# Kernel tuning notes

Hardware: AMD Instinct MI355X
Metric: run time of the kernel (lower is better)

Reference implementation:

```python
import jax, jax.numpy as jnp
import numpy as np

K = 20          # neighbors per point
BN_EPS = 1e-5


def setup_inputs() -> dict:
    key = jax.random.key(0)
    k0, k1, k2 = jax.random.split(key, 3)
    B, N, C_OUT, EDGE_DIM = 8, 4096, 64, 4  # edge feat = [diff(3), ||diff||(1)]
    x = jax.random.normal(k0, (B, N, 3), dtype=jnp.float32)
    pos = jax.random.uniform(k1, (B, N, 3), dtype=jnp.float32)
    # shared 1x1-conv MLP params (Conv1d k=1 == per-edge linear) + BatchNorm affine
    W = jax.random.normal(k2, (C_OUT, EDGE_DIM), dtype=jnp.float32) * 0.1
    b = jnp.zeros((C_OUT,), jnp.float32)
    gamma = jnp.ones((C_OUT,), jnp.float32)
    beta = jnp.zeros((C_OUT,), jnp.float32)
    return {"x": x, "pos": pos, "W": W, "b": b, "gamma": gamma, "beta": beta}


def _knn_idx(pos, k):
    # pos: [B, N, 3] -> idx of k nearest neighbors per point, self excluded. [B, N, k]
    B, N, _ = pos.shape
    sq = jnp.sum(pos * pos, axis=-1)                                   # [B, N]
    d2 = sq[:, :, None] + sq[:, None, :] - 2.0 * jnp.einsum('bnd,bmd->bnm', pos, pos)
    d2 = d2 + jnp.eye(N, dtype=pos.dtype) * 1e10                       # exclude self-loop
    _, idx = jax.lax.top_k(-d2, k)                                     # [B, N, k]
    return idx


def _forward(pos, W, b, gamma, beta, k=K):
    idx = _knn_idx(pos, k)                                             # [B, N, k] (int, non-diff)
    nbr = jax.vmap(lambda p, i: p[i])(pos, idx)                        # gather: [B, N, k, 3]
    diff = nbr - pos[:, :, None, :]                                    # neighbor - center
    dist = jnp.sqrt(jnp.sum(diff * diff, axis=-1, keepdims=True))      # [B, N, k, 1]
    feat = jnp.concatenate([diff, dist], axis=-1)                      # [B, N, k, 4]
    # shared MLP (1x1 conv): per-edge linear
    y = jnp.einsum('bnkc,oc->bnko', feat, W) + b                       # [B, N, k, 64]
    # BatchNorm1d over all edges (training-mode batch stats), per channel
    mu = jnp.mean(y, axis=(0, 1, 2))
    var = jnp.var(y, axis=(0, 1, 2))
    y = (y - mu) * jax.lax.rsqrt(var + BN_EPS) * gamma + beta
    y = jax.nn.relu(y)
    y = jnp.where(y >= 0, y, 0.1 * y)   # leaky_relu(0.1) from source (no-op after relu, kept for fidelity)
    return jnp.mean(y, axis=2)          # mean pool over each node's k edges -> [B, N, 64]


def reference(x, pos, W, b, gamma, beta):
    # x only provides (batch_size, num_points) in the source; math uses pos.
    return _forward(pos, W, b, gamma, beta)
```

## Files before the change

kernel.cpp:

```cpp
#include <hip/hip_runtime.h>

#define NB    8
#define NP    4096
#define KNN   20
#define COUT  64
#define S     4
#define BLK   256
#define QPB   (BLK / S)
#define BPB   (NP / QPB)
#define NBLK1 (NB * BPB)
#define NBLK2 ((NB * NP * 4) / BLK)
#define NMOM  14
#define MSTR  16
#define LCAP  32
#define FBIG  3.402823466e38f

typedef unsigned long long u64;
typedef unsigned int u32;

__device__ __forceinline__ void ins20(float d, u32 mi,
                                      float* __restrict__ bd,
                                      u32* __restrict__ bi) {
#pragma unroll
    for (int j = KNN - 1; j >= 1; --j) {
        const bool sh  = d < bd[j - 1];
        const bool in_ = !sh && (d < bd[j]);
        bi[j] = sh ? bi[j - 1] : (in_ ? mi : bi[j]);
        bd[j] = fminf(fmaxf(bd[j - 1], d), bd[j]);
    }
    if (d < bd[0]) { bi[0] = mi; bd[0] = d; }
}

__device__ __forceinline__ float d2_of(const float4 c, const float4 q) {
    const float base = __fadd_rn(q.w, c.w);
    const float dot  = fmaf(q.z, c.z, fmaf(q.y, c.y, __fmul_rn(q.x, c.x)));
    return fmaf(-2.0f, dot, base);
}

__global__ __launch_bounds__(BLK, 2)
void knn_kernel(const float* __restrict__ pos,
                unsigned short* __restrict__ idx_out,
                float* __restrict__ mom) {
    __shared__ float4 sp[NP];

    const int b = blockIdx.x / BPB;
    const int t = threadIdx.x;
    const int s = t & (S - 1);
    const int n = (blockIdx.x % BPB) * QPB + (t >> 2);
    const float* pb = pos + (size_t)b * NP * 3;

    for (int i = t; i < NP; i += BLK) {
        const float x = pb[3 * i], y = pb[3 * i + 1], z = pb[3 * i + 2];
        const float csq = __fadd_rn(
            __fadd_rn(__fmul_rn(x, x), __fmul_rn(y, y)), __fmul_rn(z, z));
        sp[i] = make_float4(x, y, z, csq);
    }
    __syncthreads();

    const float4 q = sp[n];

    float sd0 = FBIG, sd1 = FBIG, sd2 = FBIG, sd3 = FBIG, sd4 = FBIG;
#pragma unroll 4
    for (int i = 0; i < NP / S; i += 4) {
        const int m = (i << 2) | s;
        const float d2 = d2_of(sp[m], q);
        if (m != n && d2 < sd4) {
            sd4 = fminf(fmaxf(sd3, d2), sd4);
            sd3 = fminf(fmaxf(sd2, d2), sd3);
            sd2 = fminf(fmaxf(sd1, d2), sd2);
            sd1 = fminf(fmaxf(sd0, d2), sd1);
            sd0 = fminf(sd0, d2);
        }
    }
    float gb = sd4;
    gb = fmaxf(gb, __shfl_xor(gb, 1));
    gb = fmaxf(gb, __shfl_xor(gb, 2));

    float bd[KNN];
    u32   bi[KNN];
#pragma unroll
    for (int j = 0; j < KNN; ++j) { bd[j] = FBIG; bi[j] = 0xFFFu; }
    u64 pidx = 0;
    int cnt = 0;

#pragma unroll 4
    for (int i = 0; i < NP / S; ++i) {
        const int m = (i << 2) | s;
        const float d2 = d2_of(sp[m], q);
        const bool acc = (d2 <= gb);
        pidx = acc ? ((pidx << 12) | (u64)(u32)m) : pidx;
        cnt += (int)acc;
        if (__ballot(cnt == 4)) {
            const u32 m3 = (u32)(pidx >> 36) & 0xFFFu;
            const u32 m2 = (u32)(pidx >> 24) & 0xFFFu;
            const u32 m1 = (u32)(pidx >> 12) & 0xFFFu;
            const u32 m0 = (u32)pidx & 0xFFFu;
            const float d3r = d2_of(sp[m3], q);
            const float d2r = d2_of(sp[m2], q);
            const float d1r = d2_of(sp[m1], q);
            const float d0r = d2_of(sp[m0], q);
            ins20((cnt >= 4 && m3 != (u32)n) ? d3r : FBIG, m3, bd, bi);
            ins20((cnt >= 3 && m2 != (u32)n) ? d2r : FBIG, m2, bd, bi);
            ins20((cnt >= 2 && m1 != (u32)n) ? d1r : FBIG, m1, bd, bi);
            ins20((cnt >= 1 && m0 != (u32)n) ? d0r : FBIG, m0, bd, bi);
            cnt = 0; pidx = 0;
            float g = bd[KNN - 1];
            g = fminf(g, __shfl_xor(g, 1));
            g = fminf(g, __shfl_xor(g, 2));
            float g4 = bd[4];
            g4 = fmaxf(g4, __shfl_xor(g4, 1));
            g4 = fmaxf(g4, __shfl_xor(g4, 2));
            gb = fminf(gb, fminf(g, g4));
        }
    }
    {
        const u32 m3 = (u32)(pidx >> 36) & 0xFFFu;
        const u32 m2 = (u32)(pidx >> 24) & 0xFFFu;
        const u32 m1 = (u32)(pidx >> 12) & 0xFFFu;
        const u32 m0 = (u32)pidx & 0xFFFu;
        const float d3r = d2_of(sp[m3], q);
        const float d2r = d2_of(sp[m2], q);
        const float d1r = d2_of(sp[m1], q);
        const float d0r = d2_of(sp[m0], q);
        ins20((cnt >= 4 && m3 != (u32)n) ? d3r : FBIG, m3, bd, bi);
        ins20((cnt >= 3 && m2 != (u32)n) ? d2r : FBIG, m2, bd, bi);
        ins20((cnt >= 2 && m1 != (u32)n) ? d1r : FBIG, m1, bd, bi);
        ins20((cnt >= 1 && m0 != (u32)n) ? d0r : FBIG, m0, bd, bi);
    }

    u64 key[LCAP];
#pragma unroll
    for (int j = 0; j < KNN; ++j) {
        u32 fb = __float_as_uint(bd[j]);
        fb ^= (u32)((int)fb >> 31) | 0x80000000u;
        key[j] = ((u64)fb << 12) | bi[j];
    }
#pragma unroll
    for (int j = KNN; j < LCAP; ++j) key[j] = ~0ull;

#pragma unroll
    for (int r = 1; r <= 2; r <<= 1) {
#pragma unroll
        for (int j = 0; j < LCAP / 2; ++j) {
            const int k2 = LCAP - 1 - j;
            const u64 pa = (u64)__shfl_xor((long long)key[k2], r);
            const u64 pc = (u64)__shfl_xor((long long)key[j],  r);
            key[j]  = key[j]  < pa ? key[j]  : pa;
            key[k2] = key[k2] < pc ? key[k2] : pc;
        }
#pragma unroll
        for (int d = 16; d >= 1; d >>= 1) {
#pragma unroll
            for (int j = 0; j < LCAP; ++j) {
                if ((j & d) == 0) {
                    const u64 x = key[j], y = key[j + d];
                    key[j]     = x < y ? x : y;
                    key[j + d] = x < y ? y : x;
                }
            }
        }
    }

    unsigned short* ip = idx_out + ((size_t)b * NP + n) * KNN;
    float s1x = 0, s1y = 0, s1z = 0, s1d = 0;
    float mxx = 0, mxy = 0, mxz = 0, mxd = 0;
    float myy = 0, myz = 0, myd = 0;
    float mzz = 0, mzd = 0, mdd = 0;
#pragma unroll
    for (int j = 0; j < KNN; ++j) {
        const int m = (int)(key[j] & 0xFFFull);
        if ((j & 3) == s) ip[j] = (unsigned short)m;
        const float4 c = sp[m];
        const float dx = __fsub_rn(c.x, q.x);
        const float dy = __fsub_rn(c.y, q.y);
        const float dz = __fsub_rn(c.z, q.z);
        const float dd = sqrtf(__fadd_rn(
            __fadd_rn(__fmul_rn(dx, dx), __fmul_rn(dy, dy)), __fmul_rn(dz, dz)));
        s1x += dx; s1y += dy; s1z += dz; s1d += dd;
        mxx += dx * dx; mxy += dx * dy; mxz += dx * dz; mxd += dx * dd;
        myy += dy * dy; myz += dy * dz; myd += dy * dd;
        mzz += dz * dz; mzd += dz * dd; mdd += dd * dd;
    }
    {
        float vals[NMOM] = {s1x, s1y, s1z, s1d,
                            mxx, mxy, mxz, mxd, myy, myz, myd, mzz, mzd, mdd};
#pragma unroll
        for (int tt = 0; tt < NMOM; ++tt) {
            float v = vals[tt];
#pragma unroll
            for (int off = 32; off > 0; off >>= 1) v += __shfl_down(v, off);
            if ((t & 63) == 0) atomicAdd(&mom[tt * MSTR], v * 0.25f);
        }
    }
}

__global__ __launch_bounds__(BLK)
void out_kernel(const float* __restrict__ pos,
                const float* __restrict__ W,
                const float* __restrict__ bias,
                const float* __restrict__ gamma,
                const float* __restrict__ beta,
                const unsigned short* __restrict__ idx_in,
                const float* __restrict__ mom,
                float* __restrict__ out) {
    __shared__ float sWp[COUT][4];
    __shared__ float sbp[COUT];

    if (threadIdx.x < COUT) {
        const int o = threadIdx.x;
        double S1[4], s2v[10];
#pragma unroll
        for (int tt = 0; tt < 4; ++tt)  S1[tt]  = (double)mom[tt * MSTR];
#pragma unroll
        for (int tt = 0; tt < 10; ++tt) s2v[tt] = (double)mom[(4 + tt) * MSTR];
        const double M = (double)NB * NP * KNN;
        double mean[4];
#pragma unroll
        for (int c = 0; c < 4; ++c) mean[c] = S1[c] / M;
        double E2[4][4];
        E2[0][0] = s2v[0]; E2[0][1] = E2[1][0] = s2v[1];
        E2[0][2] = E2[2][0] = s2v[2]; E2[0][3] = E2[3][0] = s2v[3];
        E2[1][1] = s2v[4]; E2[1][2] = E2[2][1] = s2v[5];
        E2[1][3] = E2[3][1] = s2v[6];
        E2[2][2] = s2v[7]; E2[2][3] = E2[3][2] = s2v[8];
        E2[3][3] = s2v[9];
        double w[4];
#pragma unroll
        for (int c = 0; c < 4; ++c) w[c] = (double)W[o * 4 + c];
        const double bo = (double)bias[o];
        double mu = bo;
#pragma unroll
        for (int c = 0; c < 4; ++c) mu += w[c] * mean[c];
        double var = 0.0;
#pragma unroll
        for (int c = 0; c < 4; ++c)
#pragma unroll
            for (int c2 = 0; c2 < 4; ++c2)
                var += w[c] * w[c2] * (E2[c][c2] / M - mean[c] * mean[c2]);
        const double scale = (double)gamma[o] / sqrt(var + 1e-5);
#pragma unroll
        for (int c = 0; c < 4; ++c) sWp[o][c] = (float)(w[c] * scale);
        sbp[o] = (float)((bo - mu) * scale + (double)beta[o]);
    }
    __syncthreads();

    const int t  = threadIdx.x;
    const int gq = blockIdx.x * (BLK / 4) + (t >> 2);
    const int b  = gq / NP, n = gq % NP;
    const int c0 = (t & 3) * 16;
    const float* pb = pos + (size_t)b * NP * 3;
    const float qx = pb[3 * n], qy = pb[3 * n + 1], qz = pb[3 * n + 2];

    float fx[KNN], fy[KNN], fz[KNN], fd[KNN];
    const unsigned short* ip = idx_in + (size_t)gq * KNN;
#pragma unroll
    for (int j = 0; j < KNN; ++j) {
        const int m = ip[j];
        const float dx = __fsub_rn(pb[3 * m], qx);
        const float dy = __fsub_rn(pb[3 * m + 1], qy);
        const float dz = __fsub_rn(pb[3 * m + 2], qz);
        fx[j] = dx; fy[j] = dy; fz[j] = dz;
        fd[j] = sqrtf(__fadd_rn(
            __fadd_rn(__fmul_rn(dx, dx), __fmul_rn(dy, dy)), __fmul_rn(dz, dz)));
    }

    float* ob = out + (size_t)gq * COUT + c0;
    const float inv = 1.0f / (float)KNN;
#pragma unroll
    for (int o = 0; o < 16; o += 4) {
        float acc[4];
#pragma unroll
        for (int qq = 0; qq < 4; ++qq) {
            const float w0 = sWp[c0 + o + qq][0], w1 = sWp[c0 + o + qq][1];
            const float w2 = sWp[c0 + o + qq][2], w3 = sWp[c0 + o + qq][3];
            const float bb = sbp[c0 + o + qq];
            float a = 0.f;
#pragma unroll
            for (int j = 0; j < KNN; ++j) {
                float y = fmaf(fx[j], w0,
                          fmaf(fy[j], w1, fmaf(fz[j], w2, fmaf(fd[j], w3, bb))));
                a += fmaxf(y, 0.f);
            }
            acc[qq] = a * inv;
        }
        float4 p = {acc[0], acc[1], acc[2], acc[3]};
        *reinterpret_cast<float4*>(ob + o) = p;
    }
}

extern "C" void kernel_launch(void* const* d_in, const int* in_sizes, int n_in,
                              void* d_out, int out_size, void* d_ws, size_t ws_size,
                              hipStream_t stream) {
    (void)in_sizes; (void)n_in; (void)out_size; (void)ws_size;
    const float* pos   = (const float*)d_in[1];
    const float* W     = (const float*)d_in[2];
    const float* bias  = (const float*)d_in[3];
    const float* gamma = (const float*)d_in[4];
    const float* beta  = (const float*)d_in[5];
    float* out = (float*)d_out;

    float* mom = (float*)d_ws;
    unsigned short* idxws = (unsigned short*)((char*)d_ws + 1024);

    hipMemsetAsync(mom, 0, NMOM * MSTR * sizeof(float), stream);
    knn_kernel<<<NBLK1, BLK, 0, stream>>>(pos, idxws, mom);
    out_kernel<<<NBLK2, BLK, 0, stream>>>(pos, W, bias, gamma, beta,
                                          idxws, mom, out);
}
```

Baseline: 247.5 us.

## Fuse kNN and output kernels with a global atomic grid barrier

Merges the kNN/moment kernel and the output kernel into one launch. Neighbor offsets and distances stay in registers, and all blocks wait on an atomic counter until the BN moments are complete. This removes the index buffer write and read, the second global gather and the second launch. The cost is extra register pressure and reliance on all 512 blocks being co-resident, or the spin barrier deadlocks.

```diff
diff --git a/kernel.cpp b/kernel.cpp
--- a/kernel.cpp
+++ b/kernel.cpp
@@ -9,7 +9,6 @@
 #define QPB   (BLK / S)
 #define BPB   (NP / QPB)
 #define NBLK1 (NB * BPB)
-#define NBLK2 ((NB * NP * 4) / BLK)
 #define NMOM  14
 #define MSTR  16
 #define LCAP  32
@@ -38,9 +37,14 @@
 }
 
 __global__ __launch_bounds__(BLK, 2)
-void knn_kernel(const float* __restrict__ pos,
-                unsigned short* __restrict__ idx_out,
-                float* __restrict__ mom) {
+void fused_kernel(const float* __restrict__ pos,
+                  const float* __restrict__ W,
+                  const float* __restrict__ bias,
+                  const float* __restrict__ gamma,
+                  const float* __restrict__ beta,
+                  float* __restrict__ mom,
+                  u32* __restrict__ ctr,
+                  float* __restrict__ out) {
     __shared__ float4 sp[NP];
 
     const int b = blockIdx.x / BPB;
@@ -161,7 +165,7 @@
         }
     }
 
-    unsigned short* ip = idx_out + ((size_t)b * NP + n) * KNN;
+    float fx[KNN], fy[KNN], fz[KNN], fd[KNN];
     float s1x = 0, s1y = 0, s1z = 0, s1d = 0;
     float mxx = 0, mxy = 0, mxz = 0, mxd = 0;
     float myy = 0, myz = 0, myd = 0;
@@ -169,13 +173,13 @@
 #pragma unroll
     for (int j = 0; j < KNN; ++j) {
         const int m = (int)(key[j] & 0xFFFull);
-        if ((j & 3) == s) ip[j] = (unsigned short)m;
         const float4 c = sp[m];
         const float dx = __fsub_rn(c.x, q.x);
         const float dy = __fsub_rn(c.y, q.y);
         const float dz = __fsub_rn(c.z, q.z);
         const float dd = sqrtf(__fadd_rn(
             __fadd_rn(__fmul_rn(dx, dx), __fmul_rn(dy, dy)), __fmul_rn(dz, dz)));
+        fx[j] = dx; fy[j] = dy; fz[j] = dz; fd[j] = dd;
         s1x += dx; s1y += dy; s1z += dz; s1d += dd;
         mxx += dx * dx; mxy += dx * dy; mxz += dx * dz; mxd += dx * dd;
         myy += dy * dy; myz += dy * dz; myd += dy * dd;
@@ -192,27 +196,32 @@
             if ((t & 63) == 0) atomicAdd(&mom[tt * MSTR], v * 0.25f);
         }
     }
-}
-
-__global__ __launch_bounds__(BLK)
-void out_kernel(const float* __restrict__ pos,
-                const float* __restrict__ W,
-                const float* __restrict__ bias,
-                const float* __restrict__ gamma,
-                const float* __restrict__ beta,
-                const unsigned short* __restrict__ idx_in,
-                const float* __restrict__ mom,
-                float* __restrict__ out) {
-    __shared__ float sWp[COUT][4];
-    __shared__ float sbp[COUT];
-
-    if (threadIdx.x < COUT) {
-        const int o = threadIdx.x;
+
+    __syncthreads();
+    __threadfence();
+    if (t == 0) {
+        __hip_atomic_fetch_add(ctr, 1u, __ATOMIC_ACQ_REL, __HIP_MEMORY_SCOPE_AGENT);
+        while (__hip_atomic_load(ctr, __ATOMIC_ACQUIRE, __HIP_MEMORY_SCOPE_AGENT)
+               < (u32)NBLK1) {
+            __builtin_amdgcn_s_sleep(8);
+        }
+    }
+    __syncthreads();
+
+    float* lds = (float*)sp;
+    float (*sWp)[4] = (float(*)[4])lds;
+    float*  sbp     = lds + COUT * 4;
+    if (t < COUT) {
+        const int o = t;
         double S1[4], s2v[10];
 #pragma unroll
-        for (int tt = 0; tt < 4; ++tt)  S1[tt]  = (double)mom[tt * MSTR];
-#pragma unroll
-        for (int tt = 0; tt < 10; ++tt) s2v[tt] = (double)mom[(4 + tt) * MSTR];
+        for (int tt = 0; tt < 4; ++tt)
+            S1[tt] = (double)__hip_atomic_load(&mom[tt * MSTR],
+                         __ATOMIC_RELAXED, __HIP_MEMORY_SCOPE_AGENT);
+#pragma unroll
+        for (int tt = 0; tt < 10; ++tt)
+            s2v[tt] = (double)__hip_atomic_load(&mom[(4 + tt) * MSTR],
+                          __ATOMIC_RELAXED, __HIP_MEMORY_SCOPE_AGENT);
         const double M = (double)NB * NP * KNN;
         double mean[4];
 #pragma unroll
@@ -244,27 +253,8 @@
     }
     __syncthreads();
 
-    const int t  = threadIdx.x;
-    const int gq = blockIdx.x * (BLK / 4) + (t >> 2);
-    const int b  = gq / NP, n = gq % NP;
-    const int c0 = (t & 3) * 16;
-    const float* pb = pos + (size_t)b * NP * 3;
-    const float qx = pb[3 * n], qy = pb[3 * n + 1], qz = pb[3 * n + 2];
-
-    float fx[KNN], fy[KNN], fz[KNN], fd[KNN];
-    const unsigned short* ip = idx_in + (size_t)gq * KNN;
-#pragma unroll
-    for (int j = 0; j < KNN; ++j) {
-        const int m = ip[j];
-        const float dx = __fsub_rn(pb[3 * m], qx);
-        const float dy = __fsub_rn(pb[3 * m + 1], qy);
-        const float dz = __fsub_rn(pb[3 * m + 2], qz);
-        fx[j] = dx; fy[j] = dy; fz[j] = dz;
-        fd[j] = sqrtf(__fadd_rn(
-            __fadd_rn(__fmul_rn(dx, dx), __fmul_rn(dy, dy)), __fmul_rn(dz, dz)));
-    }
-
-    float* ob = out + (size_t)gq * COUT + c0;
+    const int c0 = s * 16;
+    float* ob = out + ((size_t)b * NP + n) * COUT + c0;
     const float inv = 1.0f / (float)KNN;
 #pragma unroll
     for (int o = 0; o < 16; o += 4) {
@@ -300,10 +290,9 @@
     float* out = (float*)d_out;
 
     float* mom = (float*)d_ws;
-    unsigned short* idxws = (unsigned short*)((char*)d_ws + 1024);
-
-    hipMemsetAsync(mom, 0, NMOM * MSTR * sizeof(float), stream);
-    knn_kernel<<<NBLK1, BLK, 0, stream>>>(pos, idxws, mom);
-    out_kernel<<<NBLK2, BLK, 0, stream>>>(pos, W, bias, gamma, beta,
-                                          idxws, mom, out);
-}
+    u32*   ctr = (u32*)((char*)d_ws + 960);
+
+    hipMemsetAsync(d_ws, 0, 1024, stream);
+    fused_kernel<<<NBLK1, BLK, 0, stream>>>(pos, W, bias, gamma, beta,
+                                            mom, ctr, out);
+}
```

Result: slower. 281.8 us (+13.9%).

## Bucket points by x-coordinate and restrict kNN scan to a slab window

Applied to the files above, without the earlier changes.

Adds a per-batch counting sort that buckets points into 64 slabs along x and writes sorted float4 positions, original indices and bucket offsets. The kNN kernel takes an upper bound on the 20th-neighbor distance from a strided sample pass, then scans only the buckets within that radius in x instead of all 4096 candidates. Keys now pack distance, original index and sorted slot into one 64-bit value so insertion sorts a single array. This adds an extra launch and global round trip, and the sort kernel runs on only 8 blocks.

```diff
diff --git a/kernel.cpp b/kernel.cpp
--- a/kernel.cpp
+++ b/kernel.cpp
@@ -10,25 +10,25 @@
 #define BPB   (NP / QPB)
 #define NBLK1 (NB * BPB)
 #define NBLK2 ((NB * NP * 4) / BLK)
+#define NBKT  64
 #define NMOM  14
 #define MSTR  16
 #define LCAP  32
 #define FBIG  3.402823466e38f
+#define KBIG  ((u64)0xFF7FFFFFull << 24 | 0xFFFFFFull)
 
 typedef unsigned long long u64;
 typedef unsigned int u32;
-
-__device__ __forceinline__ void ins20(float d, u32 mi,
-                                      float* __restrict__ bd,
-                                      u32* __restrict__ bi) {
+typedef unsigned short u16;
+
+__device__ __forceinline__ void kins20(u64 k, u64* __restrict__ kbd) {
 #pragma unroll
     for (int j = KNN - 1; j >= 1; --j) {
-        const bool sh  = d < bd[j - 1];
-        const bool in_ = !sh && (d < bd[j]);
-        bi[j] = sh ? bi[j - 1] : (in_ ? mi : bi[j]);
-        bd[j] = fminf(fmaxf(bd[j - 1], d), bd[j]);
-    }
-    if (d < bd[0]) { bi[0] = mi; bd[0] = d; }
+        const bool sh  = k < kbd[j - 1];
+        const bool in_ = !sh && (k < kbd[j]);
+        kbd[j] = sh ? kbd[j - 1] : (in_ ? k : kbd[j]);
+    }
+    if (k < kbd[0]) kbd[0] = k;
 }
 
 __device__ __forceinline__ float d2_of(const float4 c, const float4 q) {
@@ -37,11 +37,73 @@
     return fmaf(-2.0f, dot, base);
 }
 
+__device__ __forceinline__ u64 mk_key(float d, u32 orig, u32 ms) {
+    u32 fb = __float_as_uint(d);
+    fb ^= (u32)((int)fb >> 31) | 0x80000000u;
+    return ((u64)fb << 24) | ((u64)orig << 12) | (u64)ms;
+}
+__device__ __forceinline__ float kdist(u64 k) {
+    u32 v = (u32)(k >> 24);
+    v = (v & 0x80000000u) ? (v ^ 0x80000000u) : ~v;
+    return __uint_as_float(v);
+}
+
+__global__ __launch_bounds__(BLK)
+void sort_kernel(const float* __restrict__ pos,
+                 float4* __restrict__ f4o,
+                 u16* __restrict__ idxo,
+                 u32* __restrict__ bstart) {
+    __shared__ u32 hist[NBKT];
+    __shared__ u32 base[NBKT + 1];
+    const int b = blockIdx.x;
+    const int t = threadIdx.x;
+    const float* pb = pos + (size_t)b * NP * 3;
+
+    if (t < NBKT) hist[t] = 0;
+    __syncthreads();
+
+    float px[NP / BLK], py[NP / BLK], pz[NP / BLK];
+    int   bu[NP / BLK];
+#pragma unroll
+    for (int k = 0; k < NP / BLK; ++k) {
+        const int i = t + k * BLK;
+        px[k] = pb[3 * i]; py[k] = pb[3 * i + 1]; pz[k] = pb[3 * i + 2];
+        int bb = (int)(px[k] * (float)NBKT);
+        bb = bb < 0 ? 0 : (bb > NBKT - 1 ? NBKT - 1 : bb);
+        bu[k] = bb;
+        atomicAdd(&hist[bb], 1u);
+    }
+    __syncthreads();
+    if (t == 0) {
+        u32 acc = 0;
+#pragma unroll
+        for (int j = 0; j < NBKT; ++j) { base[j] = acc; acc += hist[j]; }
+        base[NBKT] = acc;
+    }
+    __syncthreads();
+    if (t < NBKT) hist[t] = base[t];
+    __syncthreads();
+#pragma unroll
+    for (int k = 0; k < NP / BLK; ++k) {
+        const u32 p = atomicAdd(&hist[bu[k]], 1u);
+        const float csq = __fadd_rn(__fadd_rn(__fmul_rn(px[k], px[k]),
+                          __fmul_rn(py[k], py[k])), __fmul_rn(pz[k], pz[k]));
+        f4o[(size_t)b * NP + p]  = make_float4(px[k], py[k], pz[k], csq);
+        idxo[(size_t)b * NP + p] = (u16)(t + k * BLK);
+    }
+    if (t <= NBKT) bstart[b * (NBKT + 1) + t] = base[t];
+}
+
 __global__ __launch_bounds__(BLK, 2)
 void knn_kernel(const float* __restrict__ pos,
+                const float4* __restrict__ f4in,
+                const u16* __restrict__ idxin,
+                const u32* __restrict__ bstart,
                 unsigned short* __restrict__ idx_out,
                 float* __restrict__ mom) {
-    __shared__ float4 sp[NP];
+    __shared__ float4 sp[NP + 4];
+    __shared__ u16 sidx[NP];
+    __shared__ u32 sb[NBKT + 1];
 
     const int b = blockIdx.x / BPB;
     const int t = threadIdx.x;
@@ -49,22 +111,24 @@
     const int n = (blockIdx.x % BPB) * QPB + (t >> 2);
     const float* pb = pos + (size_t)b * NP * 3;
 
-    for (int i = t; i < NP; i += BLK) {
-        const float x = pb[3 * i], y = pb[3 * i + 1], z = pb[3 * i + 2];
-        const float csq = __fadd_rn(
-            __fadd_rn(__fmul_rn(x, x), __fmul_rn(y, y)), __fmul_rn(z, z));
-        sp[i] = make_float4(x, y, z, csq);
-    }
-    __syncthreads();
-
-    const float4 q = sp[n];
+    for (int i = t; i < NP; i += BLK) sp[i] = f4in[(size_t)b * NP + i];
+    if (t < 4) sp[NP + t] = make_float4(0.f, 0.f, 0.f, 0.f);
+    for (int i = t; i < NP / 2; i += BLK)
+        ((u32*)sidx)[i] = ((const u32*)(idxin + (size_t)b * NP))[i];
+    if (t <= NBKT) sb[t] = bstart[b * (NBKT + 1) + t];
+    __syncthreads();
+
+    const float qx = pb[3 * n], qy = pb[3 * n + 1], qz = pb[3 * n + 2];
+    const float qsq = __fadd_rn(
+        __fadd_rn(__fmul_rn(qx, qx), __fmul_rn(qy, qy)), __fmul_rn(qz, qz));
+    const float4 q = make_float4(qx, qy, qz, qsq);
 
     float sd0 = FBIG, sd1 = FBIG, sd2 = FBIG, sd3 = FBIG, sd4 = FBIG;
 #pragma unroll 4
     for (int i = 0; i < NP / S; i += 4) {
         const int m = (i << 2) | s;
         const float d2 = d2_of(sp[m], q);
-        if (m != n && d2 < sd4) {
+        if (sidx[m] != (u16)n && d2 < sd4) {
             sd4 = fminf(fmaxf(sd3, d2), sd4);
             sd3 = fminf(fmaxf(sd2, d2), sd3);
             sd2 = fminf(fmaxf(sd1, d2), sd2);
@@ -76,18 +140,24 @@
     gb = fmaxf(gb, __shfl_xor(gb, 1));
     gb = fmaxf(gb, __shfl_xor(gb, 2));
 
-    float bd[KNN];
-    u32   bi[KNN];
-#pragma unroll
-    for (int j = 0; j < KNN; ++j) { bd[j] = FBIG; bi[j] = 0xFFFu; }
+    const float r = sqrtf(__fadd_rn(gb, 1e-4f));
+    int bl = (int)(__fsub_rn(qx, r) * (float)NBKT);
+    int bh = (int)(__fadd_rn(qx, r) * (float)NBKT);
+    bl = bl < 0 ? 0 : bl;  bh = bh > NBKT - 1 ? NBKT - 1 : bh;
+    const int lo = (int)sb[bl], hi = (int)sb[bh + 1];
+    const int nit = (hi - lo + S - 1) >> 2;
+
+    u64 kbd[KNN];
+#pragma unroll
+    for (int j = 0; j < KNN; ++j) kbd[j] = KBIG;
     u64 pidx = 0;
     int cnt = 0;
 
 #pragma unroll 4
-    for (int i = 0; i < NP / S; ++i) {
-        const int m = (i << 2) | s;
+    for (int k = 0; k < nit; ++k) {
+        const int m = lo + (k << 2) + s;
         const float d2 = d2_of(sp[m], q);
-        const bool acc = (d2 <= gb);
+        const bool acc = (m < hi) && (d2 <= gb);
         pidx = acc ? ((pidx << 12) | (u64)(u32)m) : pidx;
         cnt += (int)acc;
         if (__ballot(cnt == 4)) {
@@ -95,19 +165,22 @@
             const u32 m2 = (u32)(pidx >> 24) & 0xFFFu;
             const u32 m1 = (u32)(pidx >> 12) & 0xFFFu;
             const u32 m0 = (u32)pidx & 0xFFFu;
-            const float d3r = d2_of(sp[m3], q);
-            const float d2r = d2_of(sp[m2], q);
-            const float d1r = d2_of(sp[m1], q);
-            const float d0r = d2_of(sp[m0], q);
-            ins20((cnt >= 4 && m3 != (u32)n) ? d3r : FBIG, m3, bd, bi);
-            ins20((cnt >= 3 && m2 != (u32)n) ? d2r : FBIG, m2, bd, bi);
-            ins20((cnt >= 2 && m1 != (u32)n) ? d1r : FBIG, m1, bd, bi);
-            ins20((cnt >= 1 && m0 != (u32)n) ? d0r : FBIG, m0, bd, bi);
+            const u32 o3 = sidx[m3], o2 = sidx[m2], o1 = sidx[m1], o0 = sidx[m0];
+            const u64 k3 = (cnt >= 4 && o3 != (u32)n)
+                               ? mk_key(d2_of(sp[m3], q), o3, m3) : KBIG;
+            const u64 k2 = (cnt >= 3 && o2 != (u32)n)
+                               ? mk_key(d2_of(sp[m2], q), o2, m2) : KBIG;
+            const u64 k1 = (cnt >= 2 && o1 != (u32)n)
+                               ? mk_key(d2_of(sp[m1], q), o1, m1) : KBIG;
+            const u64 k0 = (cnt >= 1 && o0 != (u32)n)
+                               ? mk_key(d2_of(sp[m0], q), o0, m0) : KBIG;
+            kins20(k3, kbd); kins20(k2, kbd);
+            kins20(k1, kbd); kins20(k0, kbd);
             cnt = 0; pidx = 0;
-            float g = bd[KNN - 1];
+            float g = kdist(kbd[KNN - 1]);
             g = fminf(g, __shfl_xor(g, 1));
             g = fminf(g, __shfl_xor(g, 2));
-            float g4 = bd[4];
+            float g4 = kdist(kbd[4]);
             g4 = fmaxf(g4, __shfl_xor(g4, 1));
             g4 = fmaxf(g4, __shfl_xor(g4, 2));
             gb = fminf(gb, fminf(g, g4));
@@ -118,35 +191,33 @@
         const u32 m2 = (u32)(pidx >> 24) & 0xFFFu;
         const u32 m1 = (u32)(pidx >> 12) & 0xFFFu;
         const u32 m0 = (u32)pidx & 0xFFFu;
-        const float d3r = d2_of(sp[m3], q);
-        const float d2r = d2_of(sp[m2], q);
-        const float d1r = d2_of(sp[m1], q);
-        const float d0r = d2_of(sp[m0], q);
-        ins20((cnt >= 4 && m3 != (u32)n) ? d3r : FBIG, m3, bd, bi);
-        ins20((cnt >= 3 && m2 != (u32)n) ? d2r : FBIG, m2, bd, bi);
-        ins20((cnt >= 2 && m1 != (u32)n) ? d1r : FBIG, m1, bd, bi);
-        ins20((cnt >= 1 && m0 != (u32)n) ? d0r : FBIG, m0, bd, bi);
+        const u32 o3 = sidx[m3], o2 = sidx[m2], o1 = sidx[m1], o0 = sidx[m0];
+        const u64 k3 = (cnt >= 4 && o3 != (u32)n)
+                           ? mk_key(d2_of(sp[m3], q), o3, m3) : KBIG;
+        const u64 k2 = (cnt >= 3 && o2 != (u32)n)
+                           ? mk_key(d2_of(sp[m2], q), o2, m2) : KBIG;
+        const u64 k1 = (cnt >= 2 && o1 != (u32)n)
+                           ? mk_key(d2_of(sp[m1], q), o1, m1) : KBIG;
+        const u64 k0 = (cnt >= 1 && o0 != (u32)n)
+                           ? mk_key(d2_of(sp[m0], q), o0, m0) : KBIG;
+        kins20(k3, kbd); kins20(k2, kbd); kins20(k1, kbd); kins20(k0, kbd);
     }
 
     u64 key[LCAP];
 #pragma unroll
-    for (int j = 0; j < KNN; ++j) {
-        u32 fb = __float_as_uint(bd[j]);
-        fb ^= (u32)((int)fb >> 31) | 0x80000000u;
-        key[j] = ((u64)fb << 12) | bi[j];
-    }
-#pragma unroll
-    for (int j = KNN; j < LCAP; ++j) key[j] = ~0ull;
-
-#pragma unroll
-    for (int r = 1; r <= 2; r <<= 1) {
+    for (int j = 0; j < KNN; ++j) key[j] = kbd[j];
+#pragma unroll
+    for (int j = KNN; j < LCAP; ++j) key[j] = KBIG;
+
+#pragma unroll
+    for (int r2 = 1; r2 <= 2; r2 <<= 1) {
 #pragma unroll
         for (int j = 0; j < LCAP / 2; ++j) {
-            const int k2 = LCAP - 1 - j;
-            const u64 pa = (u64)__shfl_xor((long long)key[k2], r);
-            const u64 pc = (u64)__shfl_xor((long long)key[j],  r);
-            key[j]  = key[j]  < pa ? key[j]  : pa;
-            key[k2] = key[k2] < pc ? key[k2] : pc;
+            const int k2i = LCAP - 1 - j;
+            const u64 pa = (u64)__shfl_xor((long long)key[k2i], r2);
+            const u64 pc = (u64)__shfl_xor((long long)key[j],  r2);
+            key[j]   = key[j]   < pa ? key[j]   : pa;
+            key[k2i] = key[k2i] < pc ? key[k2i] : pc;
         }
 #pragma unroll
         for (int d = 16; d >= 1; d >>= 1) {
@@ -168,9 +239,10 @@
     float mzz = 0, mzd = 0, mdd = 0;
 #pragma unroll
     for (int j = 0; j < KNN; ++j) {
-        const int m = (int)(key[j] & 0xFFFull);
-        if ((j & 3) == s) ip[j] = (unsigned short)m;
-        const float4 c = sp[m];
+        const int ms = (int)(key[j] & 0xFFFull);
+        const int og = (int)((key[j] >> 12) & 0xFFFull);
+        if ((j & 3) == s) ip[j] = (unsigned short)og;
+        const float4 c = sp[ms];
         const float dx = __fsub_rn(c.x, q.x);
         const float dy = __fsub_rn(c.y, q.y);
         const float dz = __fsub_rn(c.z, q.z);
@@ -299,11 +371,15 @@
     const float* beta  = (const float*)d_in[5];
     float* out = (float*)d_out;
 
-    float* mom = (float*)d_ws;
-    unsigned short* idxws = (unsigned short*)((char*)d_ws + 1024);
+    float* mom   = (float*)d_ws;
+    u32*   bstart = (u32*)((char*)d_ws + 1024);
+    float4* f4s  = (float4*)((char*)d_ws + 5120);
+    u16*   sidx  = (u16*)((char*)d_ws + 5120 + (size_t)NB * NP * sizeof(float4));
+    unsigned short* idxws = (unsigned short*)((char*)sidx + (size_t)NB * NP * sizeof(u16));
 
     hipMemsetAsync(mom, 0, NMOM * MSTR * sizeof(float), stream);
-    knn_kernel<<<NBLK1, BLK, 0, stream>>>(pos, idxws, mom);
+    sort_kernel<<<NB, BLK, 0, stream>>>(pos, f4s, sidx, bstart);
+    knn_kernel<<<NBLK1, BLK, 0, stream>>>(pos, f4s, sidx, bstart, idxws, mom);
     out_kernel<<<NBLK2, BLK, 0, stream>>>(pos, W, bias, gamma, beta,
                                           idxws, mom, out);
 }
```

Result: no change. 250.1 us (+1.1%).
